# Kernel optimization log

Hardware: AMD Instinct MI355X
Metric: run time of the kernel (lower is better)

The kernel has to match this reference:

```python
import jax, jax.numpy as jnp
import numpy as np

B, C, S = 256, 1024, 14   # batch, channels, spatial (frozen by y.view(b,c,14,14))
C2 = 15                   # channels2 in the module
CAT = C // 2 * 3 + C2     # 1551 = 15 + 512 + 1024
EPS = 1e-5


def _conv(x, w, b, groups, pad):
    out = jax.lax.conv_general_dilated(
        x, w, window_strides=(1, 1), padding=((pad, pad), (pad, pad)),
        dimension_numbers=('NCHW', 'OIHW', 'NCHW'), feature_group_count=groups)
    return out + b[None, :, None, None]


def _bn(x, gamma, beta):
    # training-mode BatchNorm2d: biased batch stats over (N,H,W)
    m = x.mean((0, 2, 3), keepdims=True)
    v = x.var((0, 2, 3), keepdims=True)
    return (x - m) * jax.lax.rsqrt(v + EPS) * gamma[None, :, None, None] + beta[None, :, None, None]


def setup_inputs() -> dict:
    key = jax.random.key(0)
    ks = jax.random.split(key, 16)
    r = C2 // 7  # = 2
    inp = {
        'y': jax.random.normal(ks[0], (B, C2, S * S), jnp.float32),
        'x': jax.random.normal(ks[1], (B, C, S, S), jnp.float32),
        'fc1_w': jax.random.normal(ks[2], (r, C2), jnp.float32) * 0.2,
        'fc2_w': jax.random.normal(ks[3], (C2, r), jnp.float32) * 0.2,
        'conv_w': jax.random.normal(ks[4], (C // 2, C, 1, 1), jnp.float32) * 0.03,
        'conv_b': jnp.zeros((C // 2,), jnp.float32),
        'dconv_w': jax.random.normal(ks[5], (C, 1, 3, 3), jnp.float32) * 0.2,
        'dconv_b': jnp.zeros((C,), jnp.float32),
        'dw1_w': jax.random.normal(ks[6], (CAT, 1, 3, 3), jnp.float32) * 0.2,
        'dw1_b': jnp.zeros((CAT,), jnp.float32),
        'pw1_w': jax.random.normal(ks[7], (C // 2, CAT, 1, 1), jnp.float32) * 0.03,
        'pw1_b': jnp.zeros((C // 2,), jnp.float32),
        'gamma': jnp.ones((C // 2,), jnp.float32),
        'beta': jnp.zeros((C // 2,), jnp.float32),
        'n': 0,
    }
    return inp


def reference(y, x, fc1_w, fc2_w, conv_w, conv_b, dconv_w, dconv_b,
              dw1_w, dw1_b, pw1_w, pw1_b, gamma, beta, n):
    b = y.shape[0]
    y4 = y.reshape(b, C2, S, S)
    # SE block on the 15 sub-channels
    g = y4.mean((2, 3))                              # (b, 15) global avg pool
    h = jax.nn.relu(g @ fc1_w.T) @ fc2_w.T           # (b, 15)
    y1 = y4 * jax.nn.sigmoid(h)[:, :, None, None]
    # depthwise conv on x, then per-(b,c) row covariance of the 14x14 map
    x1 = _conv(x, dconv_w, dconv_b, C, 1)            # (b, C, 14, 14)
    x2 = jax.lax.stop_gradient(x1)                   # .detach() in the original
    xc = x2 - x2.mean(-1, keepdims=True)             # np.cov: rows=vars, cols=obs
    cov = jnp.einsum('bcik,bcjk->bcij', xc, xc) / (S - 1)
    z = _conv(cov, conv_w, conv_b, 1, 0)             # 1x1 conv C -> C//2
    z = jax.nn.sigmoid(_bn(z, gamma, beta))
    for _ in range(n):                               # n=0 at these shapes
        y1 = jax.image.resize(y1, (y1.shape[0], y1.shape[1], y1.shape[2] * 2, y1.shape[3] * 2), 'bilinear')
    cat = jnp.concatenate([y1, z, x], axis=1)        # (b, 1551, 14, 14)
    o = _conv(cat, dw1_w, dw1_b, CAT, 1)             # depthwise 3x3
    o = _conv(o, pw1_w, pw1_b, 1, 0)                 # pointwise 1x1 -> C//2
    return jax.nn.relu(_bn(o, gamma, beta))
```

## Files before the change

### kernel.cpp

```cpp
#include <hip/hip_runtime.h>

typedef unsigned int u32;
typedef unsigned short u16;
typedef __attribute__((ext_vector_type(8))) short bf16x8;
typedef __attribute__((ext_vector_type(4))) float f32x4;
typedef __attribute__((ext_vector_type(4))) u32 u32x4;

#define EPSBN 1e-5f

#define GLDS16(gp, lp) __builtin_amdgcn_global_load_lds( \
    (const __attribute__((address_space(1))) u32*)(gp), \
    (__attribute__((address_space(3))) u32*)(lp), 16, 0, 0)

#define OFF_ADW    0ull
#define OFF_COVT   0ull
#define OFF_S      160563200ull
#define OFF_WBZ    160578560ull
#define OFF_WBP    161627136ull
#define OFF_STATSZ 163265536ull
#define OFF_STATSO 163269632ull
#define OFF_SCZ    163273728ull
#define OFF_SHZ    163275776ull
#define OFF_SCO    163277824ull
#define OFF_SHO    163279872ull

static __device__ __forceinline__ float bf2f(u16 h){
  u32 u = ((u32)h) << 16; float f; __builtin_memcpy(&f, &u, 4); return f;
}
static __device__ __forceinline__ u16 f2bf(float f){
  u32 u; __builtin_memcpy(&u, &f, 4);
  u = (u + 0x7fffu + ((u >> 16) & 1u)) >> 16;
  return (u16)u;
}
static __device__ __forceinline__ u32 pk2bf(float lo, float hi){
  u32 r;
  asm("v_cvt_pk_bf16_f32 %0, %1, %2" : "=v"(r) : "v"(lo), "v"(hi));
  return r;
}

__global__ __launch_bounds__(64) void se_kernel(const float* __restrict__ y,
    const float* __restrict__ fc1, const float* __restrict__ fc2, float* __restrict__ sse){
  __shared__ float g[15];
  __shared__ float t[2];
  int b = blockIdx.x, l = threadIdx.x;
  for (int c = 0; c < 15; ++c){
    float p = 0.f;
    for (int k = l; k < 196; k += 64) p += y[((size_t)b*15 + c)*196 + k];
    p += __shfl_xor(p, 32); p += __shfl_xor(p, 16); p += __shfl_xor(p, 8);
    p += __shfl_xor(p, 4);  p += __shfl_xor(p, 2);  p += __shfl_xor(p, 1);
    if (l == 0) g[c] = p * (1.f/196.f);
  }
  __syncthreads();
  if (l < 2){
    float a = 0.f;
    for (int c = 0; c < 15; ++c) a += g[c] * fc1[l*15 + c];
    t[l] = fmaxf(a, 0.f);
  }
  __syncthreads();
  if (l < 15){
    float h = t[0]*fc2[l*2] + t[1]*fc2[l*2+1];
    sse[b*15 + l] = 1.f / (1.f + __expf(-h));
  }
}

__global__ void wconv_kernel(const float* __restrict__ cw, const float* __restrict__ pw,
                             u16* __restrict__ wbz, u16* __restrict__ wbp){
  u32 stride = gridDim.x * blockDim.x;
  for (u32 i = blockIdx.x*blockDim.x + threadIdx.x; i < 524288u; i += stride)
    wbz[i] = f2bf(cw[i]);
  for (u32 i = blockIdx.x*blockDim.x + threadIdx.x; i < 819200u; i += stride){
    u32 n = i / 1600u, k = i - n*1600u;
    wbp[i] = f2bf(k < 1551u ? pw[(size_t)n*1551 + k] : 0.f);
  }
}

__global__ __launch_bounds__(256,5) void cov_kernel(const float* __restrict__ x,
    const float* __restrict__ dcw, const float* __restrict__ dcb, u16* __restrict__ covT){
  __shared__ __align__(16) float xs[16*200];
  __shared__ __align__(16) u32 xcb[16*132];
  __shared__ float wls[16][9];
  __shared__ float wlb[16];
  u32* covL32 = (u32*)xs;

  int tid = threadIdx.x;
  int c0 = blockIdx.x * 16, b = blockIdx.y;

  {
    const float4* xg = (const float4*)(x + ((size_t)b*1024 + c0)*196);
    for (int i = tid; i < 784; i += 256){
      float4 v = xg[i];
      u32 c = (u32)i / 49u, p4 = (u32)i - c*49u;
      *(float4*)&xs[c*200u + p4*4u] = v;
    }
  }
  if (tid < 144) wls[tid/9][tid%9] = dcw[(size_t)(c0 + tid/9)*9 + (tid%9)];
  if (tid < 16) wlb[tid] = dcb[c0 + tid];
  __syncthreads();

  {
    int c = tid >> 4, i = tid & 15;
    u32 q[8];
    #pragma unroll
    for (int j = 0; j < 8; ++j) q[j] = 0u;
    if (i < 14){
      float wr[9];
      #pragma unroll
      for (int qq = 0; qq < 9; ++qq) wr[qq] = wls[c][qq];
      float topm = (i > 0) ? 1.f : 0.f, botm = (i < 13) ? 1.f : 0.f;
      wr[0] *= topm; wr[1] *= topm; wr[2] *= topm;
      wr[6] *= botm; wr[7] *= botm; wr[8] *= botm;
      float bb = wlb[c];
      float rr[3][16];
      #pragma unroll
      for (int d = 0; d < 3; ++d){
        rr[d][0] = 0.f; rr[d][15] = 0.f;
        int rowr = i + d - 1;
        rowr = rowr < 0 ? 0 : (rowr > 13 ? 13 : rowr);
        const float* src = &xs[c*200 + rowr*14];
        #pragma unroll
        for (int j = 0; j < 7; ++j)
          *(float2*)&rr[d][1 + 2*j] = *(const float2*)&src[2*j];
      }
      float ov[14];
      #pragma unroll
      for (int k = 0; k < 14; ++k){
        float a = bb;
        #pragma unroll
        for (int dy = 0; dy < 3; ++dy)
          #pragma unroll
          for (int dx = 0; dx < 3; ++dx)
            a += wr[dy*3+dx] * rr[dy][k + dx];
        ov[k] = a;
      }
      float mean = 0.f;
      #pragma unroll
      for (int k = 0; k < 14; ++k) mean += ov[k];
      mean *= (1.f/14.f);
      #pragma unroll
      for (int j = 0; j < 7; ++j)
        q[j] = pk2bf(ov[2*j] - mean, ov[2*j+1] - mean);
    }
    u32x4 q0 = {q[0], q[1], q[2], q[3]};
    u32x4 q1 = {q[4], q[5], q[6], q[7]};
    *(u32x4*)&xcb[c*132 + i*8]     = q0;
    *(u32x4*)&xcb[c*132 + i*8 + 4] = q1;
  }
  __syncthreads();

  {
    int w = tid >> 6, l = tid & 63, lr = l & 15, lq = l >> 4;
    #pragma unroll
    for (int pp = 0; pp < 2; ++pp){
      int clo = w*4 + 2*pp;
      bf16x8 alo = {0,0,0,0,0,0,0,0}, ahi = {0,0,0,0,0,0,0,0};
      if (lq < 2){
        alo = *(const bf16x8*)&xcb[clo*132 + lr*8 + lq*4];
        ahi = *(const bf16x8*)&xcb[(clo+1)*132 + lr*8 + lq*4];
      }
      f32x4 dlo = {0.f,0.f,0.f,0.f}, dhi = {0.f,0.f,0.f,0.f};
      dlo = __builtin_amdgcn_mfma_f32_16x16x32_bf16(alo, alo, dlo, 0, 0, 0);
      dhi = __builtin_amdgcn_mfma_f32_16x16x32_bf16(ahi, ahi, dhi, 0, 0, 0);
      if (lr < 14){
        int cp = w*2 + pp;
        #pragma unroll
        for (int r = 0; r < 4; ++r){
          int rowi = lq*4 + r;
          if (rowi < 14){
            u32 vv = pk2bf(dlo[r] * (1.f/13.f), dhi[r] * (1.f/13.f));
            covL32[cp*210 + rowi*14 + lr] = vv;
          }
        }
      }
    }
  }
  __syncthreads();

  for (int i = tid; i < 1568; i += 256){
    int cp = i & 7, ij = i >> 3;
    u32 v = covL32[cp*210 + ij];
    *(u32*)(covT + ((size_t)(b*196 + ij)*1024 + c0 + 2*cp)) = v;
  }
}

__global__ __launch_bounds__(256,5) void adw_kernel(
    const float* __restrict__ y, const float* __restrict__ sse,
    const u16* __restrict__ zT, const float* __restrict__ scz, const float* __restrict__ shz,
    const float* __restrict__ x, const float* __restrict__ dw1w, const float* __restrict__ dw1b,
    u16* __restrict__ Adw){
  __shared__ __align__(16) float ms[32*202];
  __shared__ float wd[32][9];
  __shared__ float bd[32];
  int tid = threadIdx.x;
  int cc0 = blockIdx.x * 32, b = blockIdx.y;

  for (int i = tid; i < 288; i += 256){
    int c = i / 9, q = i - c*9;
    int cc = cc0 + c;
    wd[c][q] = (cc < 1551) ? dw1w[(size_t)cc*9 + q] : 0.f;
  }
  if (tid < 32) bd[tid] = (cc0 + tid < 1551) ? dw1b[cc0 + tid] : 0.f;

  if (cc0 < 15){
    int ny = 15;
    for (int i = tid; i < ny*196; i += 256){
      u32 c = (u32)i / 196u, p = (u32)i - c*196u;
      ms[c*202u + p] = y[((size_t)b*15 + c)*196 + p] * sse[b*15 + c];
    }
  }
  {
    int zs = cc0 > 15 ? cc0 : 15;
    int ze = cc0 + 32 < 527 ? cc0 + 32 : 527;
    if (zs < ze){
      int nz = ze - zs, lbase = zs - cc0, obase = zs - 15;
      const u16* zrow = zT + (size_t)obase*50176 + (size_t)b*196;
      for (int i = tid; i < nz*98; i += 256){
        u32 oo = (u32)i / 98u, pp = (u32)i - oo*98u;
        u32 v = *(const u32*)(zrow + (size_t)oo*50176 + pp*2u);
        int o = obase + (int)oo;
        float s = scz[o], h = shz[o];
        float v0 = bf2f((u16)(v & 0xffffu)) * s + h;
        float v1 = bf2f((u16)(v >> 16))     * s + h;
        v0 = 1.f / (1.f + __expf(-v0));
        v1 = 1.f / (1.f + __expf(-v1));
        float2 fv = {v0, v1};
        *(float2*)&ms[(u32)(lbase + (int)oo)*202u + pp*2u] = fv;
      }
    }
  }
  {
    int xs_ = cc0 > 527 ? cc0 : 527;
    int xe = cc0 + 32 < 1551 ? cc0 + 32 : 1551;
    if (xs_ < xe){
      int nx = xe - xs_, lbase = xs_ - cc0, cxs = xs_ - 527;
      const float4* xg = (const float4*)(x + ((size_t)b*1024 + cxs)*196);
      for (int i = tid; i < nx*49; i += 256){
        float4 v = xg[i];
        u32 c = (u32)i / 49u, p4 = (u32)i - c*49u;
        float* dst = &ms[(u32)(lbase + (int)c)*202u + p4*4u];
        float2 lo = {v.x, v.y}, hi = {v.z, v.w};
        *(float2*)dst = lo;
        *(float2*)(dst + 2) = hi;
      }
    }
  }
  {
    int ps = cc0 > 1551 ? cc0 : 1551;
    int pe = cc0 + 32;
    if (ps < pe){
      int np = pe - ps, lbase = ps - cc0;
      for (int i = tid; i < np*196; i += 256){
        u32 c = (u32)i / 196u, p = (u32)i - c*196u;
        ms[(u32)(lbase + (int)c)*202u + p] = 0.f;
      }
    }
  }
  __syncthreads();

  for (int t = tid; t < 448; t += 256){
    int cc = t & 31, i = t >> 5;
    float wr[9];
    #pragma unroll
    for (int qq = 0; qq < 9; ++qq) wr[qq] = wd[cc][qq];
    float topm = (i > 0) ? 1.f : 0.f, botm = (i < 13) ? 1.f : 0.f;
    wr[0] *= topm; wr[1] *= topm; wr[2] *= topm;
    wr[6] *= botm; wr[7] *= botm; wr[8] *= botm;
    float bb = bd[cc];
    float rr[3][16];
    #pragma unroll
    for (int d = 0; d < 3; ++d){
      rr[d][0] = 0.f; rr[d][15] = 0.f;
      int rowr = i + d - 1;
      rowr = rowr < 0 ? 0 : (rowr > 13 ? 13 : rowr);
      const float* src = &ms[cc*202 + rowr*14];
      #pragma unroll
      for (int j = 0; j < 7; ++j)
        *(float2*)&rr[d][1 + 2*j] = *(const float2*)&src[2*j];
    }
    size_t obase = ((size_t)b*196 + i*14) * 1600 + cc0 + cc;
    #pragma unroll
    for (int k = 0; k < 14; ++k){
      float a = bb;
      #pragma unroll
      for (int dy = 0; dy < 3; ++dy)
        #pragma unroll
        for (int dx = 0; dx < 3; ++dx)
          a += wr[dy*3+dx] * rr[dy][k + dx];
      Adw[obase + (size_t)k*1600] = f2bf(a);
    }
  }
}

template<int MODE>
__global__ __launch_bounds__(256,2) void gemm_kernel(
    const u16* __restrict__ A, const u16* __restrict__ Bw,
    const float* __restrict__ bias, void* __restrict__ outp,
    float* __restrict__ stats, int K){
  __shared__ __align__(16) u16 lds[32768];

  int tid = threadIdx.x;
  int w = tid >> 6, l = tid & 63;
  int wm = w >> 1, wn = w & 1;
  int lr = l & 15, lq = l >> 4;
  u32 g = blockIdx.x;
  u32 lin = (g & 7u) * 196u + (g >> 3);
  int n0 = (int)(lin & 3u) * 128;
  int m0 = (int)(lin >> 2) * 128;

  f32x4 acc[4][4] = {};
  int kTiles = K >> 6;

  const u16* Abase = A  + (size_t)m0*K;
  const u16* Bbase = Bw + (size_t)n0*K;

  #pragma unroll
  for (int i = 0; i < 4; ++i){
    int s = tid + i*256;
    int row = s >> 3, c8 = s & 7, sc = c8 ^ (row & 7);
    GLDS16(Abase + (size_t)row*K + sc*8, lds + s*8);
    GLDS16(Bbase + (size_t)row*K + sc*8, lds + 8192 + s*8);
  }

  for (int kt = 0; kt < kTiles; ++kt){
    u32 bufo = (u32)(kt & 1) * 16384u;
    if (kt > 0) __builtin_amdgcn_s_barrier();
    if (kt + 1 < kTiles){
      u32 nbufo = bufo ^ 16384u;
      #pragma unroll
      for (int i = 0; i < 4; ++i){
        int s = tid + i*256;
        int row = s >> 3, c8 = s & 7, sc = c8 ^ (row & 7);
        GLDS16(Abase + (size_t)row*K + (kt+1)*64 + sc*8, lds + nbufo + s*8);
        GLDS16(Bbase + (size_t)row*K + (kt+1)*64 + sc*8, lds + nbufo + 8192 + s*8);
      }
      asm volatile("s_waitcnt vmcnt(8)" ::: "memory");
    } else {
      asm volatile("s_waitcnt vmcnt(0)" ::: "memory");
    }
    __builtin_amdgcn_s_barrier();
    asm volatile("" ::: "memory");
    const u16* Ac = lds + bufo;
    const u16* Bc = lds + bufo + 8192;
    #pragma unroll
    for (int ks = 0; ks < 2; ++ks){
      bf16x8 af[4], bfv[4];
      #pragma unroll
      for (int mi = 0; mi < 4; ++mi){
        int row = wm*64 + mi*16 + lr;
        int q = (ks*4 + lq) ^ (row & 7);
        af[mi] = *(const bf16x8*)(Ac + row*64 + q*8);
      }
      #pragma unroll
      for (int ni = 0; ni < 4; ++ni){
        int row = wn*64 + ni*16 + lr;
        int q = (ks*4 + lq) ^ (row & 7);
        bfv[ni] = *(const bf16x8*)(Bc + row*64 + q*8);
      }
      #pragma unroll
      for (int mi = 0; mi < 4; ++mi)
        #pragma unroll
        for (int ni = 0; ni < 4; ++ni)
          acc[mi][ni] = __builtin_amdgcn_mfma_f32_16x16x32_bf16(af[mi], bfv[ni], acc[mi][ni], 0, 0, 0);
    }
  }
  __syncthreads();

  #pragma unroll
  for (int ni = 0; ni < 4; ++ni){
    int col = n0 + wn*64 + ni*16 + lr;
    float bb = bias[col];
    float s1 = 0.f, s2 = 0.f;
    #pragma unroll
    for (int mi = 0; mi < 4; ++mi)
      #pragma unroll
      for (int r = 0; r < 4; ++r){
        float v = acc[mi][ni][r] + bb;
        acc[mi][ni][r] = v;
        s1 += v; s2 += v*v;
      }
    s1 += __shfl_xor(s1, 16); s1 += __shfl_xor(s1, 32);
    s2 += __shfl_xor(s2, 16); s2 += __shfl_xor(s2, 32);
    if (lq == 0){
      atomicAdd(&stats[col], s1);
      atomicAdd(&stats[512 + col], s2);
    }
  }

  float* eb = (float*)lds;
  #pragma unroll
  for (int rnd = 0; rnd < 2; ++rnd){
    if (wm == rnd){
      float* e = eb + wn * (64*65);
      #pragma unroll
      for (int mi = 0; mi < 4; ++mi)
        #pragma unroll
        for (int ni = 0; ni < 4; ++ni)
          #pragma unroll
          for (int r = 0; r < 4; ++r)
            e[(mi*16 + lq*4 + r)*65 + ni*16 + lr] = acc[mi][ni][r];
      int m = m0 + wm*64 + l;
      if (MODE == 0){
        u16* ob = (u16*)outp + (size_t)(n0 + wn*64)*50176 + m;
        #pragma unroll 8
        for (int no = 0; no < 64; ++no)
          ob[(size_t)no*50176] = f2bf(e[l*65 + no]);
      } else {
        u32 bq = (u32)m / 196u;
        u32 ij = (u32)m - bq*196u;
        float* ob = (float*)outp + ((size_t)bq*512 + n0 + wn*64)*196 + ij;
        #pragma unroll 8
        for (int no = 0; no < 64; ++no)
          ob[(size_t)no*196] = e[l*65 + no];
      }
    }
    __syncthreads();
  }
}

__global__ void bnprep_kernel(const float* __restrict__ stats, const float* __restrict__ gamma,
    const float* __restrict__ beta, float* __restrict__ sc, float* __restrict__ sh){
  int o = threadIdx.x;
  float m = stats[o] * (1.f/50176.f);
  float v = stats[512+o] * (1.f/50176.f) - m*m;
  float inv = rsqrtf(v + EPSBN);
  float g = gamma[o] * inv;
  sc[o] = g;
  sh[o] = beta[o] - m*g;
}

__global__ void final_kernel(float4* __restrict__ o4, const float* __restrict__ sc,
                             const float* __restrict__ sh){
  u32 stride = gridDim.x * blockDim.x;
  for (u32 i = blockIdx.x*blockDim.x + threadIdx.x; i < 6422528u; i += stride){
    u32 oc = (i / 49u) & 511u;
    float s = sc[oc], t = sh[oc];
    float4 v = o4[i];
    v.x = fmaxf(fmaf(v.x, s, t), 0.f);
    v.y = fmaxf(fmaf(v.y, s, t), 0.f);
    v.z = fmaxf(fmaf(v.z, s, t), 0.f);
    v.w = fmaxf(fmaf(v.w, s, t), 0.f);
    o4[i] = v;
  }
}

extern "C" void kernel_launch(void* const* d_in, const int* in_sizes, int n_in,
                              void* d_out, int out_size, void* d_ws, size_t ws_size,
                              hipStream_t stream){
  (void)in_sizes; (void)n_in; (void)out_size; (void)ws_size;
  const float* y      = (const float*)d_in[0];
  const float* x      = (const float*)d_in[1];
  const float* fc1    = (const float*)d_in[2];
  const float* fc2    = (const float*)d_in[3];
  const float* convw  = (const float*)d_in[4];
  const float* convb  = (const float*)d_in[5];
  const float* dconvw = (const float*)d_in[6];
  const float* dconvb = (const float*)d_in[7];
  const float* dw1w   = (const float*)d_in[8];
  const float* dw1b   = (const float*)d_in[9];
  const float* pw1w   = (const float*)d_in[10];
  const float* pw1b   = (const float*)d_in[11];
  const float* gamma  = (const float*)d_in[12];
  const float* beta   = (const float*)d_in[13];

  char* ws = (char*)d_ws;
  u16* covT   = (u16*)(ws + OFF_COVT);
  u16* Adw    = (u16*)(ws + OFF_ADW);
  float* sse  = (float*)(ws + OFF_S);
  u16* wbz    = (u16*)(ws + OFF_WBZ);
  u16* wbp    = (u16*)(ws + OFF_WBP);
  float* statsZ = (float*)(ws + OFF_STATSZ);
  float* statsO = (float*)(ws + OFF_STATSO);
  float* scz  = (float*)(ws + OFF_SCZ);
  float* shz  = (float*)(ws + OFF_SHZ);
  float* sco  = (float*)(ws + OFF_SCO);
  float* sho  = (float*)(ws + OFF_SHO);
  u16* zT     = (u16*)d_out;
  float* outf = (float*)d_out;

  hipMemsetAsync(statsZ, 0, 8192, stream);
  se_kernel<<<256, 64, 0, stream>>>(y, fc1, fc2, sse);
  wconv_kernel<<<2048, 256, 0, stream>>>(convw, pw1w, wbz, wbp);
  cov_kernel<<<dim3(64, 256), 256, 0, stream>>>(x, dconvw, dconvb, covT);
  gemm_kernel<0><<<1568, 256, 0, stream>>>(covT, wbz, convb, (void*)zT, statsZ, 1024);
  bnprep_kernel<<<1, 512, 0, stream>>>(statsZ, gamma, beta, scz, shz);
  adw_kernel<<<dim3(50, 256), 256, 0, stream>>>(y, sse, zT, scz, shz, x, dw1w, dw1b, Adw);
  gemm_kernel<1><<<1568, 256, 0, stream>>>(Adw, wbp, pw1b, (void*)outf, statsO, 1600);
  bnprep_kernel<<<1, 512, 0, stream>>>(statsO, gamma, beta, sco, sho);
  final_kernel<<<8192, 256, 0, stream>>>((float4*)outf, sco, sho);
}
```

Before: 497.2 us.

## Process 64 channels per cov block with double-buffered async loads and wider stores

Each cov_kernel block now handles 64 channels in four 16-channel stages. The next stage's input is prefetched into a second LDS buffer via global_load_lds while the current stage computes the conv and the MFMA covariance. The covT writeback now uses 16-byte stores of 8 channels instead of 4-byte stores, reducing store transactions. In exchange, LDS use per block grows, occupancy drops (launch bounds 5 to 2), and the grid shrinks by a factor of four.

```diff
diff --git a/kernel.cpp b/kernel.cpp
--- a/kernel.cpp
+++ b/kernel.cpp
@@ -74,100 +74,117 @@
   }
 }
 
-__global__ __launch_bounds__(256,5) void cov_kernel(const float* __restrict__ x,
+__global__ __launch_bounds__(256,2) void cov_kernel(const float* __restrict__ x,
     const float* __restrict__ dcw, const float* __restrict__ dcb, u16* __restrict__ covT){
-  __shared__ __align__(16) float xs[16*200];
+  __shared__ __align__(16) float xs[2*3136];
   __shared__ __align__(16) u32 xcb[16*132];
-  __shared__ float wls[16][9];
-  __shared__ float wlb[16];
-  u32* covL32 = (u32*)xs;
+  __shared__ __align__(16) u32 covL32[32*210];
+  __shared__ float wls[64][9];
+  __shared__ float wlb[64];
 
   int tid = threadIdx.x;
-  int c0 = blockIdx.x * 16, b = blockIdx.y;
-
-  {
-    const float4* xg = (const float4*)(x + ((size_t)b*1024 + c0)*196);
-    for (int i = tid; i < 784; i += 256){
-      float4 v = xg[i];
-      u32 c = (u32)i / 49u, p4 = (u32)i - c*49u;
-      *(float4*)&xs[c*200u + p4*4u] = v;
-    }
-  }
-  if (tid < 144) wls[tid/9][tid%9] = dcw[(size_t)(c0 + tid/9)*9 + (tid%9)];
-  if (tid < 16) wlb[tid] = dcb[c0 + tid];
-  __syncthreads();
-
-  {
-    int c = tid >> 4, i = tid & 15;
-    u32 q[8];
-    #pragma unroll
-    for (int j = 0; j < 8; ++j) q[j] = 0u;
-    if (i < 14){
-      float wr[9];
-      #pragma unroll
-      for (int qq = 0; qq < 9; ++qq) wr[qq] = wls[c][qq];
-      float topm = (i > 0) ? 1.f : 0.f, botm = (i < 13) ? 1.f : 0.f;
-      wr[0] *= topm; wr[1] *= topm; wr[2] *= topm;
-      wr[6] *= botm; wr[7] *= botm; wr[8] *= botm;
-      float bb = wlb[c];
-      float rr[3][16];
-      #pragma unroll
-      for (int d = 0; d < 3; ++d){
-        rr[d][0] = 0.f; rr[d][15] = 0.f;
-        int rowr = i + d - 1;
-        rowr = rowr < 0 ? 0 : (rowr > 13 ? 13 : rowr);
-        const float* src = &xs[c*200 + rowr*14];
+  int c0 = blockIdx.x * 64, b = blockIdx.y;
+  const float* xbase = x + ((size_t)b*1024 + c0)*196;
+
+  #pragma unroll
+  for (int i = 0; i < 3; ++i){
+    int s = tid + i*256;
+    GLDS16(xbase + s*4, xs + s*4);
+  }
+  if (tid < 16){ int s = tid + 768; GLDS16(xbase + s*4, xs + s*4); }
+
+  for (int i = tid; i < 576; i += 256) wls[i/9][i%9] = dcw[(size_t)(c0 + i/9)*9 + (i%9)];
+  if (tid < 64) wlb[tid] = dcb[c0 + tid];
+
+  for (int sg = 0; sg < 4; ++sg){
+    u32 xo = (u32)(sg & 1) * 3136u;
+    asm volatile("s_waitcnt vmcnt(0)" ::: "memory");
+    __builtin_amdgcn_s_barrier();
+    asm volatile("" ::: "memory");
+
+    {
+      int c = tid >> 4, i = tid & 15;
+      int cg = sg*16 + c;
+      u32 q[8];
+      #pragma unroll
+      for (int j = 0; j < 8; ++j) q[j] = 0u;
+      if (i < 14){
+        float wr[9];
+        #pragma unroll
+        for (int qq = 0; qq < 9; ++qq) wr[qq] = wls[cg][qq];
+        float topm = (i > 0) ? 1.f : 0.f, botm = (i < 13) ? 1.f : 0.f;
+        wr[0] *= topm; wr[1] *= topm; wr[2] *= topm;
+        wr[6] *= botm; wr[7] *= botm; wr[8] *= botm;
+        float bb = wlb[cg];
+        float rr[3][16];
+        #pragma unroll
+        for (int d = 0; d < 3; ++d){
+          rr[d][0] = 0.f; rr[d][15] = 0.f;
+          int rowr = i + d - 1;
+          rowr = rowr < 0 ? 0 : (rowr > 13 ? 13 : rowr);
+          const float* src = &xs[xo + c*196 + rowr*14];
+          #pragma unroll
+          for (int j = 0; j < 7; ++j)
+            *(float2*)&rr[d][1 + 2*j] = *(const float2*)&src[2*j];
+        }
+        float ov[14];
+        #pragma unroll
+        for (int k = 0; k < 14; ++k){
+          float a = bb;
+          #pragma unroll
+          for (int dy = 0; dy < 3; ++dy)
+            #pragma unroll
+            for (int dx = 0; dx < 3; ++dx)
+              a += wr[dy*3+dx] * rr[dy][k + dx];
+          ov[k] = a;
+        }
+        float mean = 0.f;
+        #pragma unroll
+        for (int k = 0; k < 14; ++k) mean += ov[k];
+        mean *= (1.f/14.f);
         #pragma unroll
         for (int j = 0; j < 7; ++j)
-          *(float2*)&rr[d][1 + 2*j] = *(const float2*)&src[2*j];
-      }
-      float ov[14];
-      #pragma unroll
-      for (int k = 0; k < 14; ++k){
-        float a = bb;
-        #pragma unroll
-        for (int dy = 0; dy < 3; ++dy)
+          q[j] = pk2bf(ov[2*j] - mean, ov[2*j+1] - mean);
+      }
+      u32x4 q0 = {q[0], q[1], q[2], q[3]};
+      u32x4 q1 = {q[4], q[5], q[6], q[7]};
+      *(u32x4*)&xcb[c*132 + i*8]     = q0;
+      *(u32x4*)&xcb[c*132 + i*8 + 4] = q1;
+    }
+    __builtin_amdgcn_s_barrier();
+    if (sg < 3){
+      const float* nsrc = xbase + (size_t)(sg+1)*3136;
+      u32 xo2 = xo ^ 3136u;
+      #pragma unroll
+      for (int i = 0; i < 3; ++i){
+        int s = tid + i*256;
+        GLDS16(nsrc + s*4, xs + xo2 + s*4);
+      }
+      if (tid < 16){ int s = tid + 768; GLDS16(nsrc + s*4, xs + xo2 + s*4); }
+    }
+
+    {
+      int w = tid >> 6, l = tid & 63, lr = l & 15, lq = l >> 4;
+      #pragma unroll
+      for (int pp = 0; pp < 2; ++pp){
+        int clo = w*4 + 2*pp;
+        bf16x8 alo = {0,0,0,0,0,0,0,0}, ahi = {0,0,0,0,0,0,0,0};
+        if (lq < 2){
+          alo = *(const bf16x8*)&xcb[clo*132 + lr*8 + lq*4];
+          ahi = *(const bf16x8*)&xcb[(clo+1)*132 + lr*8 + lq*4];
+        }
+        f32x4 dlo = {0.f,0.f,0.f,0.f}, dhi = {0.f,0.f,0.f,0.f};
+        dlo = __builtin_amdgcn_mfma_f32_16x16x32_bf16(alo, alo, dlo, 0, 0, 0);
+        dhi = __builtin_amdgcn_mfma_f32_16x16x32_bf16(ahi, ahi, dhi, 0, 0, 0);
+        if (lr < 14){
+          int cp = sg*8 + w*2 + pp;
           #pragma unroll
-          for (int dx = 0; dx < 3; ++dx)
-            a += wr[dy*3+dx] * rr[dy][k + dx];
-        ov[k] = a;
-      }
-      float mean = 0.f;
-      #pragma unroll
-      for (int k = 0; k < 14; ++k) mean += ov[k];
-      mean *= (1.f/14.f);
-      #pragma unroll
-      for (int j = 0; j < 7; ++j)
-        q[j] = pk2bf(ov[2*j] - mean, ov[2*j+1] - mean);
-    }
-    u32x4 q0 = {q[0], q[1], q[2], q[3]};
-    u32x4 q1 = {q[4], q[5], q[6], q[7]};
-    *(u32x4*)&xcb[c*132 + i*8]     = q0;
-    *(u32x4*)&xcb[c*132 + i*8 + 4] = q1;
-  }
-  __syncthreads();
-
-  {
-    int w = tid >> 6, l = tid & 63, lr = l & 15, lq = l >> 4;
-    #pragma unroll
-    for (int pp = 0; pp < 2; ++pp){
-      int clo = w*4 + 2*pp;
-      bf16x8 alo = {0,0,0,0,0,0,0,0}, ahi = {0,0,0,0,0,0,0,0};
-      if (lq < 2){
-        alo = *(const bf16x8*)&xcb[clo*132 + lr*8 + lq*4];
-        ahi = *(const bf16x8*)&xcb[(clo+1)*132 + lr*8 + lq*4];
-      }
-      f32x4 dlo = {0.f,0.f,0.f,0.f}, dhi = {0.f,0.f,0.f,0.f};
-      dlo = __builtin_amdgcn_mfma_f32_16x16x32_bf16(alo, alo, dlo, 0, 0, 0);
-      dhi = __builtin_amdgcn_mfma_f32_16x16x32_bf16(ahi, ahi, dhi, 0, 0, 0);
-      if (lr < 14){
-        int cp = w*2 + pp;
-        #pragma unroll
-        for (int r = 0; r < 4; ++r){
-          int rowi = lq*4 + r;
-          if (rowi < 14){
-            u32 vv = pk2bf(dlo[r] * (1.f/13.f), dhi[r] * (1.f/13.f));
-            covL32[cp*210 + rowi*14 + lr] = vv;
+          for (int r = 0; r < 4; ++r){
+            int rowi = lq*4 + r;
+            if (rowi < 14){
+              u32 vv = pk2bf(dlo[r] * (1.f/13.f), dhi[r] * (1.f/13.f));
+              covL32[cp*210 + rowi*14 + lr] = vv;
+            }
           }
         }
       }
@@ -176,9 +193,13 @@
   __syncthreads();
 
   for (int i = tid; i < 1568; i += 256){
-    int cp = i & 7, ij = i >> 3;
-    u32 v = covL32[cp*210 + ij];
-    *(u32*)(covT + ((size_t)(b*196 + ij)*1024 + c0 + 2*cp)) = v;
+    int g = i & 7, ij = i >> 3;
+    u32x4 v;
+    v.x = covL32[(g*4+0)*210 + ij];
+    v.y = covL32[(g*4+1)*210 + ij];
+    v.z = covL32[(g*4+2)*210 + ij];
+    v.w = covL32[(g*4+3)*210 + ij];
+    *(u32x4*)(covT + ((size_t)(b*196 + ij)*1024 + c0 + g*8)) = v;
   }
 }
 
@@ -479,7 +500,7 @@
   hipMemsetAsync(statsZ, 0, 8192, stream);
   se_kernel<<<256, 64, 0, stream>>>(y, fc1, fc2, sse);
   wconv_kernel<<<2048, 256, 0, stream>>>(convw, pw1w, wbz, wbp);
-  cov_kernel<<<dim3(64, 256), 256, 0, stream>>>(x, dconvw, dconvb, covT);
+  cov_kernel<<<dim3(16, 256), 256, 0, stream>>>(x, dconvw, dconvb, covT);
   gemm_kernel<0><<<1568, 256, 0, stream>>>(covT, wbz, convb, (void*)zT, statsZ, 1024);
   bnprep_kernel<<<1, 512, 0, stream>>>(statsZ, gamma, beta, scz, shz);
   adw_kernel<<<dim3(50, 256), 256, 0, stream>>>(y, sse, zT, scz, shz, x, dw1w, dw1b, Adw);
```

Result: faster. 485.6 us (-2.3%).
